# Optimization experiments

Hardware: AMD Instinct MI355X
Metric: run time of the kernel (lower is better)

## Reference

```python
import jax, jax.numpy as jnp
import numpy as np

N = 100000       # nodes
E = 1600000      # edges (before self loops)
G = 64           # graphs in batch
IN, HID, OUT = 128, 64, 16
NEG_SLOPE = 0.2  # PyG GATConv default


def setup_inputs() -> dict:
    key = jax.random.key(0)
    ks = jax.random.split(key, 16)
    s = 0.1  # weight init scale
    return {
        "x": jax.random.normal(ks[0], (N, IN), dtype=jnp.float32),
        "edge_index": jax.random.randint(ks[1], (2, E), 0, N, dtype=jnp.int32),
        "batch": jnp.sort(jax.random.randint(ks[2], (N,), 0, G, dtype=jnp.int32)),
        "W1": jax.random.normal(ks[3], (IN, 2 * HID), dtype=jnp.float32) * s,
        "a_src1": jax.random.normal(ks[4], (2, HID), dtype=jnp.float32) * s,
        "a_dst1": jax.random.normal(ks[5], (2, HID), dtype=jnp.float32) * s,
        "b1": jax.random.normal(ks[6], (2 * HID,), dtype=jnp.float32) * s,
        "W2": jax.random.normal(ks[7], (2 * HID, HID), dtype=jnp.float32) * s,
        "a_src2": jax.random.normal(ks[8], (1, HID), dtype=jnp.float32) * s,
        "a_dst2": jax.random.normal(ks[9], (1, HID), dtype=jnp.float32) * s,
        "b2": jax.random.normal(ks[10], (HID,), dtype=jnp.float32) * s,
        "dw1": jax.random.normal(ks[11], (HID, HID), dtype=jnp.float32) * s,
        "db1": jax.random.normal(ks[12], (HID,), dtype=jnp.float32) * s,
        "dw2": jax.random.normal(ks[13], (HID, OUT), dtype=jnp.float32) * s,
        "db2": jax.random.normal(ks[14], (OUT,), dtype=jnp.float32) * s,
    }


def gat_conv(x, src, dst, W, a_src, a_dst, b):
    """PyG GATConv (concat=True, self-loops already appended to src/dst)."""
    n = x.shape[0]
    heads, out = a_src.shape
    h = (x @ W).reshape(n, heads, out)                       # [N,H,O]
    e_src = jnp.einsum("nho,ho->nh", h, a_src)               # [N,H]
    e_dst = jnp.einsum("nho,ho->nh", h, a_dst)
    e = jax.nn.leaky_relu(e_src[src] + e_dst[dst], NEG_SLOPE)  # [E',H]
    # segment softmax over incoming edges of each destination node
    m = jax.lax.stop_gradient(jax.ops.segment_max(e, dst, num_segments=n))
    a = jnp.exp(e - m[dst])
    denom = jax.ops.segment_sum(a, dst, num_segments=n)
    alpha = a / denom[dst]                                   # [E',H]
    msg = h[src] * alpha[:, :, None]                         # [E',H,O]
    agg = jax.ops.segment_sum(msg, dst, num_segments=n)      # [N,H,O]
    return agg.reshape(n, heads * out) + b


def reference(x, edge_index, batch, W1, a_src1, a_dst1, b1, W2, a_src2, a_dst2,
              b2, dw1, db1, dw2, db2):
    n = x.shape[0]
    loops = jnp.arange(n, dtype=edge_index.dtype)            # add_self_loops=True
    src = jnp.concatenate([edge_index[0], loops])
    dst = jnp.concatenate([edge_index[1], loops])

    h = jax.nn.relu(gat_conv(x, src, dst, W1, a_src1, a_dst1, b1))   # [N,128]
    h = gat_conv(h, src, dst, W2, a_src2, a_dst2, b2)                # [N,64]

    # global mean pool over graphs
    cnt = jax.ops.segment_sum(jnp.ones((n,), h.dtype), batch, num_segments=G)
    pooled = jax.ops.segment_sum(h, batch, num_segments=G)
    pooled = pooled / jnp.maximum(cnt, 1.0)[:, None]                  # [G,64]

    # decoder MLP (dropout inactive in eval)
    z = jax.nn.relu(pooled @ dw1 + db1)
    return z @ dw2 + db2                                              # [G,16]
```

## Files before the change

### kernel.cpp

```cpp
#include <hip/hip_runtime.h>
#include <stdint.h>


#define LRELU(x) ((x) > 0.f ? (x) : 0.2f * (x))
#define LOG2E 1.4426950408889634f
#define BCAP 3072

typedef short bf8 __attribute__((ext_vector_type(8)));
typedef float f32x4 __attribute__((ext_vector_type(4)));
typedef float f32x2 __attribute__((ext_vector_type(2)));

__device__ __forceinline__ uint16_t f2bf(float f) {
  uint32_t u = __float_as_uint(f);
  u += 0x7fff + ((u >> 16) & 1);
  return (uint16_t)(u >> 16);
}
__device__ __forceinline__ uint32_t pack2bf(float a, float b) {
  return (uint32_t)f2bf(a) | ((uint32_t)f2bf(b) << 16);
}
__device__ __forceinline__ uint8_t f2fp8(float v) {
  return (uint8_t)(__builtin_amdgcn_cvt_pk_fp8_f32(v, v, 0, false) & 0xff);
}
__device__ __forceinline__ void fp8x4_to_f32(uint32_t v, float* o) {
  f32x2 lo = __builtin_amdgcn_cvt_pk_f32_fp8(v, false);
  f32x2 hi = __builtin_amdgcn_cvt_pk_f32_fp8(v, true);
  o[0] = lo[0]; o[1] = lo[1]; o[2] = hi[0]; o[3] = hi[1];
}


__global__ __launch_bounds__(256) void scatter_cvt_kernel(
    const int* __restrict__ ei, int* __restrict__ bcur,
    uint32_t* __restrict__ bpack, const float* __restrict__ W1,
    const float* __restrict__ W2, uint16_t* __restrict__ WT1,
    uint16_t* __restrict__ WT2, int E, int E2, int shift, int nb, int gCH) {
  int blk = blockIdx.x;
  int t = threadIdx.x;
  if (blk >= gCH) {
    int idx = (blk - gCH) * 256 + t;
    if (idx < 128 * 128) {
      int n = idx >> 7, k = idx & 127;
      WT1[idx] = f2bf(W1[(size_t)k * 128 + n]);
    } else if (idx < 128 * 128 + 64 * 128) {
      int j = idx - 128 * 128;
      int n = j >> 7, k = j & 127;
      WT2[j] = f2bf(W2[(size_t)k * 64 + n]);
    }
    return;
  }
  __shared__ int lh[1024];
  __shared__ int lb[1024];
  for (int i = t; i < 1024; i += 256) lh[i] = 0;
  __syncthreads();
  int base = blk * 4096;
  int bszm1 = (1 << shift) - 1;
  uint32_t pk[16];
  int rk[16], bk[16];
#pragma unroll
  for (int u = 0; u < 16; ++u) {
    int e = base + u * 256 + t;
    if (e < E2) {
      int s, d;
      if (e < E) { s = ei[e]; d = ei[E + e]; } else { s = d = e - E; }
      bk[u] = d >> shift;
      pk[u] = ((uint32_t)s << shift) | (uint32_t)(d & bszm1);
      rk[u] = atomicAdd(&lh[bk[u]], 1);
    } else rk[u] = -1;
  }
  __syncthreads();
  for (int i = t; i < nb; i += 256) {
    int c = lh[i];
    lb[i] = c ? atomicAdd(&bcur[i], c) : 0;
  }
  __syncthreads();
#pragma unroll
  for (int u = 0; u < 16; ++u) {
    if (rk[u] >= 0) {
      int pos = lb[bk[u]] + rk[u];
      if (pos < BCAP) bpack[(size_t)bk[u] * BCAP + pos] = pk[u];
    }
  }
}


__device__ __forceinline__ void bfinal_body(const uint32_t* __restrict__ bpack,
                                            const int* __restrict__ bcur,
                                            int2* __restrict__ off2,
                                            int* __restrict__ ssrc, int N,
                                            int shift, int b) {
  __shared__ int hist[512];
  __shared__ int loff[512];
  __shared__ int ssc[256];
  __shared__ int lsrc[BCAP];
  int t = threadIdx.x;
  int bsz = 1 << shift;
  int node0 = b << shift;
  int e0 = b * BCAP;
  int cnt = min(bcur[b], BCAP);
  for (int i = t; i < bsz; i += 256) hist[i] = 0;
  __syncthreads();
  uint32_t pe[12];
  int ne = 0;
#pragma unroll
  for (int j = 0; j < 12; ++j) {
    int i = j * 256 + t;
    if (i < cnt) { pe[j] = bpack[(size_t)b * BCAP + i]; ne = j + 1; }
  }
  int bszm1 = bsz - 1;
  for (int j = 0; j < ne; ++j) atomicAdd(&hist[pe[j] & bszm1], 1);
  __syncthreads();
  int per = (bsz + 255) >> 8;
  int basei = t * per;
  int va[2] = {0, 0};
  int sum = 0;
#pragma unroll 2
  for (int j = 0; j < per; ++j) {
    if (basei + j < bsz) va[j] = hist[basei + j];
    sum += va[j];
  }
  ssc[t] = sum;
  __syncthreads();
  for (int d = 1; d < 256; d <<= 1) {
    int x = (t >= d) ? ssc[t - d] : 0;
    __syncthreads();
    ssc[t] += x;
    __syncthreads();
  }
  int run = ssc[t] - sum;
#pragma unroll 2
  for (int j = 0; j < per; ++j) {
    if (basei + j < bsz) {
      loff[basei + j] = run;
      int v = node0 + basei + j;
      if (v < N) off2[v] = make_int2(e0 + run, e0 + run + va[j]);
      run += va[j];
    }
  }
  for (int i = t; i < bsz; i += 256) hist[i] = 0;
  __syncthreads();
  for (int j = 0; j < ne; ++j) {
    int ld = pe[j] & bszm1;
    int r = atomicAdd(&hist[ld], 1);
    lsrc[loff[ld] + r] = (int)(pe[j] >> shift);
  }
  __syncthreads();
  for (int i = t; i < cnt; i += 256) ssrc[e0 + i] = lsrc[i];
}


template <int N, int HEADS, int AFP32>
__device__ __forceinline__ void gemm_body(const void* __restrict__ Av,
                                          const uint16_t* __restrict__ WT,
                                          uint8_t* __restrict__ C,
                                          const float* __restrict__ aS,
                                          const float* __restrict__ aD,
                                          float* __restrict__ es,
                                          float* __restrict__ ed, int M, int blk) {
  constexpr int CT = N / 16;
  int wave = threadIdx.x >> 6;
  int lane = threadIdx.x & 63;
  int m16 = lane & 15;
  int quad = lane >> 4;
  int row_base = blk * 128 + wave * 32;
  if (row_base >= M) return;
  const uint16_t* Ab0 = (const uint16_t*)Av + (size_t)(row_base + m16) * 128;
  const uint16_t* Ab1 = Ab0 + (size_t)16 * 128;
  const float* Af0 = (const float*)Av + (size_t)(row_base + m16) * 128;
  const float* Af1 = Af0 + (size_t)16 * 128;
  f32x4 acc[2][CT] = {};
#pragma unroll
  for (int ks = 0; ks < 4; ++ks) {
    int k0 = ks * 32 + quad * 8;
    bf8 a0, a1;
    if (AFP32) {
      float4 v0 = *reinterpret_cast<const float4*>(Af0 + k0);
      float4 v1 = *reinterpret_cast<const float4*>(Af0 + k0 + 4);
      uint4 pk0;
      pk0.x = pack2bf(v0.x, v0.y); pk0.y = pack2bf(v0.z, v0.w);
      pk0.z = pack2bf(v1.x, v1.y); pk0.w = pack2bf(v1.z, v1.w);
      a0 = *reinterpret_cast<bf8*>(&pk0);
      float4 w0 = *reinterpret_cast<const float4*>(Af1 + k0);
      float4 w1 = *reinterpret_cast<const float4*>(Af1 + k0 + 4);
      uint4 pk1;
      pk1.x = pack2bf(w0.x, w0.y); pk1.y = pack2bf(w0.z, w0.w);
      pk1.z = pack2bf(w1.x, w1.y); pk1.w = pack2bf(w1.z, w1.w);
      a1 = *reinterpret_cast<bf8*>(&pk1);
    } else {
      a0 = *reinterpret_cast<const bf8*>(Ab0 + k0);
      a1 = *reinterpret_cast<const bf8*>(Ab1 + k0);
    }
#pragma unroll
    for (int c = 0; c < CT; ++c) {
      bf8 b = *reinterpret_cast<const bf8*>(WT + (size_t)(c * 16 + m16) * 128 + k0);
      acc[0][c] = __builtin_amdgcn_mfma_f32_16x16x32_bf16(a0, b, acc[0][c], 0, 0, 0);
      acc[1][c] = __builtin_amdgcn_mfma_f32_16x16x32_bf16(a1, b, acc[1][c], 0, 0, 0);
    }
  }
#pragma unroll
  for (int r = 0; r < 2; ++r) {
#pragma unroll
    for (int c = 0; c < CT; ++c) {
#pragma unroll
      for (int reg = 0; reg < 4; ++reg) {
        int row = row_base + r * 16 + quad * 4 + reg;
        C[(size_t)row * N + c * 16 + m16] = f2fp8(acc[r][c][reg]);
      }
    }
  }
  float aSv[CT], aDv[CT];
#pragma unroll
  for (int c = 0; c < CT; ++c) {
    aSv[c] = aS[c * 16 + m16];
    aDv[c] = aD[c * 16 + m16];
  }
#pragma unroll
  for (int r = 0; r < 2; ++r) {
#pragma unroll
    for (int reg = 0; reg < 4; ++reg) {
      float es0 = 0.f, es1 = 0.f, ed0 = 0.f, ed1 = 0.f;
#pragma unroll
      for (int c = 0; c < CT; ++c) {
        float v = acc[r][c][reg];
        if (HEADS == 2 && c >= CT / 2) {
          es1 = fmaf(v, aSv[c], es1);
          ed1 = fmaf(v, aDv[c], ed1);
        } else {
          es0 = fmaf(v, aSv[c], es0);
          ed0 = fmaf(v, aDv[c], ed0);
        }
      }
#pragma unroll
      for (int o = 1; o < 16; o <<= 1) {
        es0 += __shfl_xor(es0, o);
        ed0 += __shfl_xor(ed0, o);
        if (HEADS == 2) {
          es1 += __shfl_xor(es1, o);
          ed1 += __shfl_xor(ed1, o);
        }
      }
      if (m16 == 0) {
        int row = row_base + r * 16 + quad * 4 + reg;
        if (HEADS == 2) {
          es[row * 2] = es0 * LOG2E; es[row * 2 + 1] = es1 * LOG2E;
          ed[row * 2] = ed0 * LOG2E; ed[row * 2 + 1] = ed1 * LOG2E;
        } else {
          es[row] = es0 * LOG2E;
          ed[row] = ed0 * LOG2E;
        }
      }
    }
  }
}


__global__ __launch_bounds__(256) void gemm1_bfinal_kernel(
    const float* __restrict__ x, const uint16_t* __restrict__ WT1,
    uint8_t* __restrict__ hb1, const float* __restrict__ aS,
    const float* __restrict__ aD, float* __restrict__ es, float* __restrict__ ed,
    int M, const uint32_t* __restrict__ bpack, const int* __restrict__ bcur,
    int2* __restrict__ off2, int* __restrict__ ssrc, int shift, int gM) {
  int blk = blockIdx.x;
  if (blk < gM) {
    gemm_body<128, 2, 1>(x, WT1, hb1, aS, aD, es, ed, M, blk);
  } else {
    bfinal_body(bpack, bcur, off2, ssrc, M, shift, blk - gM);
  }
}

template <int N, int HEADS, int AFP32>
__global__ __launch_bounds__(256) void gemm_mfma(const void* __restrict__ Av,
                                                 const uint16_t* __restrict__ WT,
                                                 uint8_t* __restrict__ C,
                                                 const float* __restrict__ aS,
                                                 const float* __restrict__ aD,
                                                 float* __restrict__ es,
                                                 float* __restrict__ ed, int M) {
  gemm_body<N, HEADS, AFP32>(Av, WT, C, aS, aD, es, ed, M, blockIdx.x);
}


__global__ void agg1_kernel(const uint2* __restrict__ h8, const float* __restrict__ es,
                            const float2* __restrict__ ed, const int2* __restrict__ off2,
                            const int* __restrict__ ssrc, const float* __restrict__ b,
                            uint4* __restrict__ outb4, int n) {
  int w = __builtin_amdgcn_readfirstlane((blockIdx.x * 256 + threadIdx.x) >> 6);
  int lane = threadIdx.x & 63;
  if (w >= n) return;
  int sub = lane >> 4;
  int q = lane & 15;
  bool hi = q >= 8;
  float2 edw = ed[w];
  float edh = hi ? edw.y : edw.x;
  const float* esp = es + (hi ? 1 : 0);
  float acc[8] = {};
  float den = 0.f;
  int2 oo = off2[w];
  int e0 = oo.x, e1 = oo.y;
  int base = e0;
  for (; base + 8 <= e1; base += 8) {
    int s0 = ssrc[base + sub];
    int s1 = ssrc[base + 4 + sub];
    float ev0 = esp[2 * s0];
    float ev1 = esp[2 * s1];
    uint2 g0 = h8[(size_t)s0 * 16 + q];
    uint2 g1 = h8[(size_t)s1 * 16 + q];
    float a0 = exp2f(LRELU(ev0 + edh));
    float a1 = exp2f(LRELU(ev1 + edh));
    den += a0 + a1;
    float f0[8], f1[8];
    fp8x4_to_f32(g0.x, f0); fp8x4_to_f32(g0.y, f0 + 4);
    fp8x4_to_f32(g1.x, f1); fp8x4_to_f32(g1.y, f1 + 4);
#pragma unroll
    for (int j = 0; j < 8; ++j) acc[j] = fmaf(a0, f0[j], acc[j]);
#pragma unroll
    for (int j = 0; j < 8; ++j) acc[j] = fmaf(a1, f1[j], acc[j]);
  }
  if (base + 4 <= e1) {
    int s0 = ssrc[base + sub];
    float ev0 = esp[2 * s0];
    uint2 g0 = h8[(size_t)s0 * 16 + q];
    float a0 = exp2f(LRELU(ev0 + edh));
    den += a0;
    float f0[8];
    fp8x4_to_f32(g0.x, f0); fp8x4_to_f32(g0.y, f0 + 4);
#pragma unroll
    for (int j = 0; j < 8; ++j) acc[j] = fmaf(a0, f0[j], acc[j]);
    base += 4;
  }
  int e = base + sub;
  if (e < e1) {
    int s0 = ssrc[e];
    float ev0 = esp[2 * s0];
    uint2 g0 = h8[(size_t)s0 * 16 + q];
    float a0 = exp2f(LRELU(ev0 + edh));
    den += a0;
    float f0[8];
    fp8x4_to_f32(g0.x, f0); fp8x4_to_f32(g0.y, f0 + 4);
#pragma unroll
    for (int j = 0; j < 8; ++j) acc[j] = fmaf(a0, f0[j], acc[j]);
  }
#pragma unroll
  for (int m = 16; m <= 32; m <<= 1) {
    den += __shfl_xor(den, m);
#pragma unroll
    for (int j = 0; j < 8; ++j) acc[j] += __shfl_xor(acc[j], m);
  }
  if (sub == 0) {
    float inv = 1.0f / den;
    float4 b0 = reinterpret_cast<const float4*>(b)[q * 2];
    float4 b1 = reinterpret_cast<const float4*>(b)[q * 2 + 1];
    float o0 = fmaxf(fmaf(acc[0], inv, b0.x), 0.f);
    float o1 = fmaxf(fmaf(acc[1], inv, b0.y), 0.f);
    float o2 = fmaxf(fmaf(acc[2], inv, b0.z), 0.f);
    float o3 = fmaxf(fmaf(acc[3], inv, b0.w), 0.f);
    float o4 = fmaxf(fmaf(acc[4], inv, b1.x), 0.f);
    float o5 = fmaxf(fmaf(acc[5], inv, b1.y), 0.f);
    float o6 = fmaxf(fmaf(acc[6], inv, b1.z), 0.f);
    float o7 = fmaxf(fmaf(acc[7], inv, b1.w), 0.f);
    uint4 o;
    o.x = pack2bf(o0, o1);
    o.y = pack2bf(o2, o3);
    o.z = pack2bf(o4, o5);
    o.w = pack2bf(o6, o7);
    outb4[(size_t)w * 16 + q] = o;
  }
}


__global__ void agg2_pool_kernel(const uint32_t* __restrict__ h8,
                                 const float* __restrict__ es,
                                 const float* __restrict__ ed,
                                 const int2* __restrict__ off2,
                                 const int* __restrict__ ssrc,
                                 const float* __restrict__ b,
                                 const int* __restrict__ batch,
                                 float* __restrict__ pooled, int n) {
  int w = __builtin_amdgcn_readfirstlane((blockIdx.x * 256 + threadIdx.x) >> 6);
  int wave = threadIdx.x >> 6;
  int lane = threadIdx.x & 63;
  bool act = (w < n);
  int sub = lane >> 4;
  int q = lane & 15;
  __shared__ float red[4][64];
  __shared__ int gidS[4];
  float acc[4] = {};
  float den = 1.f;
  if (act) {
    float edw = ed[w];
    den = 0.f;
    int2 oo = off2[w];
    int e0 = oo.x, e1 = oo.y;
    int base = e0;
    for (; base + 8 <= e1; base += 8) {
      int s0 = ssrc[base + sub];
      int s1 = ssrc[base + 4 + sub];
      float ev0 = es[s0];
      float ev1 = es[s1];
      uint32_t g0 = h8[(size_t)s0 * 16 + q];
      uint32_t g1 = h8[(size_t)s1 * 16 + q];
      float a0 = exp2f(LRELU(ev0 + edw));
      float a1 = exp2f(LRELU(ev1 + edw));
      den += a0 + a1;
      float f0[4], f1[4];
      fp8x4_to_f32(g0, f0);
      fp8x4_to_f32(g1, f1);
#pragma unroll
      for (int j = 0; j < 4; ++j) acc[j] = fmaf(a0, f0[j], acc[j]);
#pragma unroll
      for (int j = 0; j < 4; ++j) acc[j] = fmaf(a1, f1[j], acc[j]);
    }
    if (base + 4 <= e1) {
      int s0 = ssrc[base + sub];
      float ev0 = es[s0];
      uint32_t g0 = h8[(size_t)s0 * 16 + q];
      float a0 = exp2f(LRELU(ev0 + edw));
      den += a0;
      float f0[4];
      fp8x4_to_f32(g0, f0);
#pragma unroll
      for (int j = 0; j < 4; ++j) acc[j] = fmaf(a0, f0[j], acc[j]);
      base += 4;
    }
    int e = base + sub;
    if (e < e1) {
      int s0 = ssrc[e];
      float ev0 = es[s0];
      uint32_t g0 = h8[(size_t)s0 * 16 + q];
      float a0 = exp2f(LRELU(ev0 + edw));
      den += a0;
      float f0[4];
      fp8x4_to_f32(g0, f0);
#pragma unroll
      for (int j = 0; j < 4; ++j) acc[j] = fmaf(a0, f0[j], acc[j]);
    }
#pragma unroll
    for (int m = 16; m <= 32; m <<= 1) {
      den += __shfl_xor(den, m);
#pragma unroll
      for (int j = 0; j < 4; ++j) acc[j] += __shfl_xor(acc[j], m);
    }
    if (sub == 0) {
      float inv = 1.0f / den;
      float4 bb = reinterpret_cast<const float4*>(b)[q];
      red[wave][q * 4 + 0] = fmaf(acc[0], inv, bb.x);
      red[wave][q * 4 + 1] = fmaf(acc[1], inv, bb.y);
      red[wave][q * 4 + 2] = fmaf(acc[2], inv, bb.z);
      red[wave][q * 4 + 3] = fmaf(acc[3], inv, bb.w);
    }
  }
  if (lane == 0) gidS[wave] = act ? batch[w] : -1;
  __syncthreads();
  int g0 = gidS[0];
  bool uni = (g0 >= 0) & (gidS[1] == g0) & (gidS[2] == g0) & (gidS[3] == g0);
  int t = threadIdx.x;
  if (uni) {
    if (t < 64) {
      float s = red[0][t] + red[1][t] + red[2][t] + red[3][t];
      atomicAdd(&pooled[g0 * 64 + t], s);
    }
  } else {
    int wv = t >> 6, c = t & 63;
    int g = gidS[wv];
    if (g >= 0) atomicAdd(&pooled[g * 64 + c], red[wv][c]);
  }
}


__device__ __forceinline__ int lowerb(const int* __restrict__ a, int n, int v) {
  int lo = 0, hi = n;
  while (lo < hi) {
    int mid = (lo + hi) >> 1;
    if (a[mid] < v) lo = mid + 1; else hi = mid;
  }
  return lo;
}

__global__ void mlp_kernel(const float* __restrict__ pooled,
                           const int* __restrict__ batch, int n,
                           const float* __restrict__ dw1, const float* __restrict__ db1,
                           const float* __restrict__ dw2, const float* __restrict__ db2,
                           float* __restrict__ out) {
  int g = blockIdx.x;
  int c = threadIdx.x;
  __shared__ float P[64];
  __shared__ float Z[64];
  __shared__ int cntS;
  if (c == 0) cntS = lowerb(batch, n, g + 1) - lowerb(batch, n, g);
  __syncthreads();
  float inv = 1.0f / fmaxf((float)cntS, 1.0f);
  P[c] = pooled[g * 64 + c] * inv;
  __syncthreads();
  float s = db1[c];
#pragma unroll
  for (int k = 0; k < 64; ++k) s = fmaf(P[k], dw1[k * 64 + c], s);
  Z[c] = fmaxf(s, 0.f);
  __syncthreads();
  if (c < 16) {
    float s2 = db2[c];
#pragma unroll
    for (int k = 0; k < 64; ++k) s2 = fmaf(Z[k], dw2[k * 16 + c], s2);
    out[g * 16 + c] = s2;
  }
}


extern "C" void kernel_launch(void* const* d_in, const int* in_sizes, int n_in,
                              void* d_out, int out_size, void* d_ws, size_t ws_size,
                              hipStream_t stream) {
  const float* x      = (const float*)d_in[0];
  const int*   ei     = (const int*)d_in[1];
  const int*   batch  = (const int*)d_in[2];
  const float* W1     = (const float*)d_in[3];
  const float* a_src1 = (const float*)d_in[4];
  const float* a_dst1 = (const float*)d_in[5];
  const float* b1     = (const float*)d_in[6];
  const float* W2     = (const float*)d_in[7];
  const float* a_src2 = (const float*)d_in[8];
  const float* a_dst2 = (const float*)d_in[9];
  const float* b2     = (const float*)d_in[10];
  const float* dw1    = (const float*)d_in[11];
  const float* db1    = (const float*)d_in[12];
  const float* dw2    = (const float*)d_in[13];
  const float* db2    = (const float*)d_in[14];
  float* out = (float*)d_out;

  const int N = in_sizes[2];
  const int E = in_sizes[1] / 2;
  const int E2 = E + N;
  const int G = out_size / 16;

  int shift = 7;
  while ((N >> shift) >= 1024) ++shift;
  const int NB = ((N - 1) >> shift) + 1;

  char* ws = (char*)d_ws;
  size_t o = 0;
  auto alloc = [&](size_t bytes) {
    void* p = ws + o;
    o = (o + bytes + 255) & ~(size_t)255;
    return p;
  };
  int*      zreg   = (int*)alloc((size_t)(1024 + G * 64) * 4);
  int*      bcur   = zreg;
  float*    pooled = (float*)(zreg + 1024);
  int2*     off2   = (int2*)alloc((size_t)N * 8);
  uint32_t* bpack  = (uint32_t*)alloc((size_t)NB * BCAP * 4);
  int*      ssrc   = (int*)alloc((size_t)NB * BCAP * 4);
  float*    es1    = (float*)alloc((size_t)N * 2 * 4);
  float*    ed1    = (float*)alloc((size_t)N * 2 * 4);
  float*    es2    = (float*)alloc((size_t)N * 4);
  float*    ed2    = (float*)alloc((size_t)N * 4);
  uint16_t* wt1b   = (uint16_t*)alloc((size_t)128 * 128 * 2);
  uint16_t* wt2b   = (uint16_t*)alloc((size_t)64 * 128 * 2);
  uint8_t*  hb1    = (uint8_t*)alloc((size_t)N * 128);
  uint8_t*  hb2    = (uint8_t*)alloc((size_t)N * 64);
  uint32_t* out1b  = (uint32_t*)alloc((size_t)N * 64 * 4);

  hipMemsetAsync(zreg, 0, (size_t)(1024 + G * 64) * 4, stream);

  int gM   = (N + 127) / 128;
  int gW   = (N + 3) / 4;
  int gCH  = (E2 + 4095) / 4096;
  int gCVT = (128 * 128 + 64 * 128 + 255) / 256;

  scatter_cvt_kernel<<<gCH + gCVT, 256, 0, stream>>>(ei, bcur, bpack, W1, W2,
                                                     wt1b, wt2b, E, E2, shift,
                                                     NB, gCH);
  gemm1_bfinal_kernel<<<gM + NB, 256, 0, stream>>>(x, wt1b, hb1, a_src1, a_dst1,
                                                   es1, ed1, N, bpack, bcur,
                                                   off2, ssrc, shift, gM);
  agg1_kernel<<<gW, 256, 0, stream>>>((const uint2*)hb1, es1,
                                      (const float2*)ed1, off2, ssrc, b1,
                                      (uint4*)out1b, N);
  gemm_mfma<64, 1, 0><<<gM, 256, 0, stream>>>((const void*)out1b, wt2b, hb2,
                                              a_src2, a_dst2, es2, ed2, N);
  agg2_pool_kernel<<<gW, 256, 0, stream>>>((const uint32_t*)hb2, es2, ed2, off2,
                                           ssrc, b2, batch, pooled, N);
  mlp_kernel<<<G, 64, 0, stream>>>(pooled, batch, N, dw1, db1, dw2, db2, out);
}
```

Measured before the change: 312.7 us.

## Widen per-lane gathers in aggregation kernels and slice pooled atomics

Both aggregation kernels now use 8 lanes per edge with 16-byte (layer 1) or 8-byte (layer 2) fp8 gathers, so each wave processes 8 edges at once instead of 4 and issues fewer, wider loads. The pooled sum is spread across 8 slices indexed by block id, which cuts atomic contention on the 64x64 accumulator, and the MLP kernel adds the slices back together. In exchange each lane holds more accumulator registers, the shuffle reduction takes one more step, and the memset and final pooled read grow eightfold.

```diff
diff --git a/kernel.cpp b/kernel.cpp
--- a/kernel.cpp
+++ b/kernel.cpp
@@ -5,6 +5,7 @@
 #define LRELU(x) ((x) > 0.f ? (x) : 0.2f * (x))
 #define LOG2E 1.4426950408889634f
 #define BCAP 3072
+#define PSLICE 8
 
 typedef short bf8 __attribute__((ext_vector_type(8)));
 typedef float f32x4 __attribute__((ext_vector_type(4)));
@@ -278,111 +279,115 @@
 }
 
 
-__global__ void agg1_kernel(const uint2* __restrict__ h8, const float* __restrict__ es,
+__global__ void agg1_kernel(const uint4* __restrict__ h16, const float* __restrict__ es,
                             const float2* __restrict__ ed, const int2* __restrict__ off2,
                             const int* __restrict__ ssrc, const float* __restrict__ b,
                             uint4* __restrict__ outb4, int n) {
   int w = __builtin_amdgcn_readfirstlane((blockIdx.x * 256 + threadIdx.x) >> 6);
   int lane = threadIdx.x & 63;
   if (w >= n) return;
-  int sub = lane >> 4;
-  int q = lane & 15;
-  bool hi = q >= 8;
+  int sub = lane >> 3;
+  int q = lane & 7;
+  bool hi = q >= 4;
   float2 edw = ed[w];
   float edh = hi ? edw.y : edw.x;
   const float* esp = es + (hi ? 1 : 0);
-  float acc[8] = {};
+  float acc[16] = {};
   float den = 0.f;
   int2 oo = off2[w];
   int e0 = oo.x, e1 = oo.y;
   int base = e0;
-  for (; base + 8 <= e1; base += 8) {
+  for (; base + 16 <= e1; base += 16) {
     int s0 = ssrc[base + sub];
-    int s1 = ssrc[base + 4 + sub];
+    int s1 = ssrc[base + 8 + sub];
     float ev0 = esp[2 * s0];
     float ev1 = esp[2 * s1];
-    uint2 g0 = h8[(size_t)s0 * 16 + q];
-    uint2 g1 = h8[(size_t)s1 * 16 + q];
+    uint4 g0 = h16[(size_t)s0 * 8 + q];
+    uint4 g1 = h16[(size_t)s1 * 8 + q];
     float a0 = exp2f(LRELU(ev0 + edh));
     float a1 = exp2f(LRELU(ev1 + edh));
     den += a0 + a1;
-    float f0[8], f1[8];
+    float f0[16], f1[16];
     fp8x4_to_f32(g0.x, f0); fp8x4_to_f32(g0.y, f0 + 4);
+    fp8x4_to_f32(g0.z, f0 + 8); fp8x4_to_f32(g0.w, f0 + 12);
     fp8x4_to_f32(g1.x, f1); fp8x4_to_f32(g1.y, f1 + 4);
-#pragma unroll
-    for (int j = 0; j < 8; ++j) acc[j] = fmaf(a0, f0[j], acc[j]);
-#pragma unroll
-    for (int j = 0; j < 8; ++j) acc[j] = fmaf(a1, f1[j], acc[j]);
-  }
-  if (base + 4 <= e1) {
+    fp8x4_to_f32(g1.z, f1 + 8); fp8x4_to_f32(g1.w, f1 + 12);
+#pragma unroll
+    for (int j = 0; j < 16; ++j) acc[j] = fmaf(a0, f0[j], acc[j]);
+#pragma unroll
+    for (int j = 0; j < 16; ++j) acc[j] = fmaf(a1, f1[j], acc[j]);
+  }
+  if (base + 8 <= e1) {
     int s0 = ssrc[base + sub];
     float ev0 = esp[2 * s0];
-    uint2 g0 = h8[(size_t)s0 * 16 + q];
+    uint4 g0 = h16[(size_t)s0 * 8 + q];
     float a0 = exp2f(LRELU(ev0 + edh));
     den += a0;
-    float f0[8];
+    float f0[16];
     fp8x4_to_f32(g0.x, f0); fp8x4_to_f32(g0.y, f0 + 4);
-#pragma unroll
-    for (int j = 0; j < 8; ++j) acc[j] = fmaf(a0, f0[j], acc[j]);
-    base += 4;
+    fp8x4_to_f32(g0.z, f0 + 8); fp8x4_to_f32(g0.w, f0 + 12);
+#pragma unroll
+    for (int j = 0; j < 16; ++j) acc[j] = fmaf(a0, f0[j], acc[j]);
+    base += 8;
   }
   int e = base + sub;
   if (e < e1) {
     int s0 = ssrc[e];
     float ev0 = esp[2 * s0];
-    uint2 g0 = h8[(size_t)s0 * 16 + q];
+    uint4 g0 = h16[(size_t)s0 * 8 + q];
     float a0 = exp2f(LRELU(ev0 + edh));
     den += a0;
-    float f0[8];
+    float f0[16];
     fp8x4_to_f32(g0.x, f0); fp8x4_to_f32(g0.y, f0 + 4);
-#pragma unroll
-    for (int j = 0; j < 8; ++j) acc[j] = fmaf(a0, f0[j], acc[j]);
-  }
-#pragma unroll
-  for (int m = 16; m <= 32; m <<= 1) {
+    fp8x4_to_f32(g0.z, f0 + 8); fp8x4_to_f32(g0.w, f0 + 12);
+#pragma unroll
+    for (int j = 0; j < 16; ++j) acc[j] = fmaf(a0, f0[j], acc[j]);
+  }
+#pragma unroll
+  for (int m = 8; m <= 32; m <<= 1) {
     den += __shfl_xor(den, m);
 #pragma unroll
-    for (int j = 0; j < 8; ++j) acc[j] += __shfl_xor(acc[j], m);
+    for (int j = 0; j < 16; ++j) acc[j] += __shfl_xor(acc[j], m);
   }
   if (sub == 0) {
     float inv = 1.0f / den;
-    float4 b0 = reinterpret_cast<const float4*>(b)[q * 2];
-    float4 b1 = reinterpret_cast<const float4*>(b)[q * 2 + 1];
-    float o0 = fmaxf(fmaf(acc[0], inv, b0.x), 0.f);
-    float o1 = fmaxf(fmaf(acc[1], inv, b0.y), 0.f);
-    float o2 = fmaxf(fmaf(acc[2], inv, b0.z), 0.f);
-    float o3 = fmaxf(fmaf(acc[3], inv, b0.w), 0.f);
-    float o4 = fmaxf(fmaf(acc[4], inv, b1.x), 0.f);
-    float o5 = fmaxf(fmaf(acc[5], inv, b1.y), 0.f);
-    float o6 = fmaxf(fmaf(acc[6], inv, b1.z), 0.f);
-    float o7 = fmaxf(fmaf(acc[7], inv, b1.w), 0.f);
-    uint4 o;
-    o.x = pack2bf(o0, o1);
-    o.y = pack2bf(o2, o3);
-    o.z = pack2bf(o4, o5);
-    o.w = pack2bf(o6, o7);
-    outb4[(size_t)w * 16 + q] = o;
-  }
-}
-
-
-__global__ void agg2_pool_kernel(const uint32_t* __restrict__ h8,
+    float o[16];
+#pragma unroll
+    for (int k = 0; k < 4; ++k) {
+      float4 bb = reinterpret_cast<const float4*>(b)[q * 4 + k];
+      o[k * 4 + 0] = fmaxf(fmaf(acc[k * 4 + 0], inv, bb.x), 0.f);
+      o[k * 4 + 1] = fmaxf(fmaf(acc[k * 4 + 1], inv, bb.y), 0.f);
+      o[k * 4 + 2] = fmaxf(fmaf(acc[k * 4 + 2], inv, bb.z), 0.f);
+      o[k * 4 + 3] = fmaxf(fmaf(acc[k * 4 + 3], inv, bb.w), 0.f);
+    }
+    uint4 oA, oB;
+    oA.x = pack2bf(o[0], o[1]);   oA.y = pack2bf(o[2], o[3]);
+    oA.z = pack2bf(o[4], o[5]);   oA.w = pack2bf(o[6], o[7]);
+    oB.x = pack2bf(o[8], o[9]);   oB.y = pack2bf(o[10], o[11]);
+    oB.z = pack2bf(o[12], o[13]); oB.w = pack2bf(o[14], o[15]);
+    outb4[(size_t)w * 16 + q * 2] = oA;
+    outb4[(size_t)w * 16 + q * 2 + 1] = oB;
+  }
+}
+
+
+__global__ void agg2_pool_kernel(const uint2* __restrict__ h8,
                                  const float* __restrict__ es,
                                  const float* __restrict__ ed,
                                  const int2* __restrict__ off2,
                                  const int* __restrict__ ssrc,
                                  const float* __restrict__ b,
                                  const int* __restrict__ batch,
-                                 float* __restrict__ pooled, int n) {
+                                 float* __restrict__ pooled, int gstride, int n) {
   int w = __builtin_amdgcn_readfirstlane((blockIdx.x * 256 + threadIdx.x) >> 6);
   int wave = threadIdx.x >> 6;
   int lane = threadIdx.x & 63;
   bool act = (w < n);
-  int sub = lane >> 4;
-  int q = lane & 15;
+  int sub = lane >> 3;
+  int q = lane & 7;
   __shared__ float red[4][64];
   __shared__ int gidS[4];
-  float acc[4] = {};
+  float acc[8] = {};
   float den = 1.f;
   if (act) {
     float edw = ed[w];
@@ -390,77 +395,83 @@
     int2 oo = off2[w];
     int e0 = oo.x, e1 = oo.y;
     int base = e0;
-    for (; base + 8 <= e1; base += 8) {
+    for (; base + 16 <= e1; base += 16) {
       int s0 = ssrc[base + sub];
-      int s1 = ssrc[base + 4 + sub];
+      int s1 = ssrc[base + 8 + sub];
       float ev0 = es[s0];
       float ev1 = es[s1];
-      uint32_t g0 = h8[(size_t)s0 * 16 + q];
-      uint32_t g1 = h8[(size_t)s1 * 16 + q];
+      uint2 g0 = h8[(size_t)s0 * 8 + q];
+      uint2 g1 = h8[(size_t)s1 * 8 + q];
       float a0 = exp2f(LRELU(ev0 + edw));
       float a1 = exp2f(LRELU(ev1 + edw));
       den += a0 + a1;
-      float f0[4], f1[4];
-      fp8x4_to_f32(g0, f0);
-      fp8x4_to_f32(g1, f1);
-#pragma unroll
-      for (int j = 0; j < 4; ++j) acc[j] = fmaf(a0, f0[j], acc[j]);
-#pragma unroll
-      for (int j = 0; j < 4; ++j) acc[j] = fmaf(a1, f1[j], acc[j]);
-    }
-    if (base + 4 <= e1) {
+      float f0[8], f1[8];
+      fp8x4_to_f32(g0.x, f0); fp8x4_to_f32(g0.y, f0 + 4);
+      fp8x4_to_f32(g1.x, f1); fp8x4_to_f32(g1.y, f1 + 4);
+#pragma unroll
+      for (int j = 0; j < 8; ++j) acc[j] = fmaf(a0, f0[j], acc[j]);
+#pragma unroll
+      for (int j = 0; j < 8; ++j) acc[j] = fmaf(a1, f1[j], acc[j]);
+    }
+    if (base + 8 <= e1) {
       int s0 = ssrc[base + sub];
       float ev0 = es[s0];
-      uint32_t g0 = h8[(size_t)s0 * 16 + q];
+      uint2 g0 = h8[(size_t)s0 * 8 + q];
       float a0 = exp2f(LRELU(ev0 + edw));
       den += a0;
-      float f0[4];
-      fp8x4_to_f32(g0, f0);
-#pragma unroll
-      for (int j = 0; j < 4; ++j) acc[j] = fmaf(a0, f0[j], acc[j]);
-      base += 4;
+      float f0[8];
+      fp8x4_to_f32(g0.x, f0); fp8x4_to_f32(g0.y, f0 + 4);
+#pragma unroll
+      for (int j = 0; j < 8; ++j) acc[j] = fmaf(a0, f0[j], acc[j]);
+      base += 8;
     }
     int e = base + sub;
     if (e < e1) {
       int s0 = ssrc[e];
       float ev0 = es[s0];
-      uint32_t g0 = h8[(size_t)s0 * 16 + q];
+      uint2 g0 = h8[(size_t)s0 * 8 + q];
       float a0 = exp2f(LRELU(ev0 + edw));
       den += a0;
-      float f0[4];
-      fp8x4_to_f32(g0, f0);
-#pragma unroll
-      for (int j = 0; j < 4; ++j) acc[j] = fmaf(a0, f0[j], acc[j]);
-    }
-#pragma unroll
-    for (int m = 16; m <= 32; m <<= 1) {
+      float f0[8];
+      fp8x4_to_f32(g0.x, f0); fp8x4_to_f32(g0.y, f0 + 4);
+#pragma unroll
+      for (int j = 0; j < 8; ++j) acc[j] = fmaf(a0, f0[j], acc[j]);
+    }
+#pragma unroll
+    for (int m = 8; m <= 32; m <<= 1) {
       den += __shfl_xor(den, m);
 #pragma unroll
-      for (int j = 0; j < 4; ++j) acc[j] += __shfl_xor(acc[j], m);
+      for (int j = 0; j < 8; ++j) acc[j] += __shfl_xor(acc[j], m);
     }
     if (sub == 0) {
       float inv = 1.0f / den;
-      float4 bb = reinterpret_cast<const float4*>(b)[q];
-      red[wave][q * 4 + 0] = fmaf(acc[0], inv, bb.x);
-      red[wave][q * 4 + 1] = fmaf(acc[1], inv, bb.y);
-      red[wave][q * 4 + 2] = fmaf(acc[2], inv, bb.z);
-      red[wave][q * 4 + 3] = fmaf(acc[3], inv, bb.w);
+      float4 b0 = reinterpret_cast<const float4*>(b)[q * 2];
+      float4 b1 = reinterpret_cast<const float4*>(b)[q * 2 + 1];
+      red[wave][q * 8 + 0] = fmaf(acc[0], inv, b0.x);
+      red[wave][q * 8 + 1] = fmaf(acc[1], inv, b0.y);
+      red[wave][q * 8 + 2] = fmaf(acc[2], inv, b0.z);
+      red[wave][q * 8 + 3] = fmaf(acc[3], inv, b0.w);
+      red[wave][q * 8 + 4] = fmaf(acc[4], inv, b1.x);
+      red[wave][q * 8 + 5] = fmaf(acc[5], inv, b1.y);
+      red[wave][q * 8 + 6] = fmaf(acc[6], inv, b1.z);
+      red[wave][q * 8 + 7] = fmaf(acc[7], inv, b1.w);
     }
   }
   if (lane == 0) gidS[wave] = act ? batch[w] : -1;
   __syncthreads();
+  float* pslice = pooled + (size_t)(blockIdx.x & (PSLICE - 1)) * gstride;
   int g0 = gidS[0];
   bool uni = (g0 >= 0) & (gidS[1] == g0) & (gidS[2] == g0) & (gidS[3] == g0);
   int t = threadIdx.x;
   if (uni) {
     if (t < 64) {
       float s = red[0][t] + red[1][t] + red[2][t] + red[3][t];
-      atomicAdd(&pooled[g0 * 64 + t], s);
+      atomicAdd(&pslice[g0 * 64 + t], s);
     }
   } else {
     int wv = t >> 6, c = t & 63;
     int g = gidS[wv];
-    if (g >= 0) atomicAdd(&pooled[g * 64 + c], red[wv][c]);
+    if (g >= 0) atomicAdd(&pslice[g * 64 + c], red[wv][c]);
   }
 }
 
@@ -474,7 +485,7 @@
   return lo;
 }
 
-__global__ void mlp_kernel(const float* __restrict__ pooled,
+__global__ void mlp_kernel(const float* __restrict__ pooled, int gstride,
                            const int* __restrict__ batch, int n,
                            const float* __restrict__ dw1, const float* __restrict__ db1,
                            const float* __restrict__ dw2, const float* __restrict__ db2,
@@ -487,7 +498,10 @@
   if (c == 0) cntS = lowerb(batch, n, g + 1) - lowerb(batch, n, g);
   __syncthreads();
   float inv = 1.0f / fmaxf((float)cntS, 1.0f);
-  P[c] = pooled[g * 64 + c] * inv;
+  float p = 0.f;
+#pragma unroll
+  for (int s = 0; s < PSLICE; ++s) p += pooled[(size_t)s * gstride + g * 64 + c];
+  P[c] = p * inv;
   __syncthreads();
   float s = db1[c];
 #pragma unroll
@@ -527,6 +541,7 @@
   const int E = in_sizes[1] / 2;
   const int E2 = E + N;
   const int G = out_size / 16;
+  const int gstride = G * 64;
 
   int shift = 7;
   while ((N >> shift) >= 1024) ++shift;
@@ -539,7 +554,7 @@
     o = (o + bytes + 255) & ~(size_t)255;
     return p;
   };
-  int*      zreg   = (int*)alloc((size_t)(1024 + G * 64) * 4);
+  int*      zreg   = (int*)alloc((size_t)(1024 + PSLICE * gstride) * 4);
   int*      bcur   = zreg;
   float*    pooled = (float*)(zreg + 1024);
   int2*     off2   = (int2*)alloc((size_t)N * 8);
@@ -555,7 +570,7 @@
   uint8_t*  hb2    = (uint8_t*)alloc((size_t)N * 64);
   uint32_t* out1b  = (uint32_t*)alloc((size_t)N * 64 * 4);
 
-  hipMemsetAsync(zreg, 0, (size_t)(1024 + G * 64) * 4, stream);
+  hipMemsetAsync(zreg, 0, (size_t)(1024 + PSLICE * gstride) * 4, stream);
 
   int gM   = (N + 127) / 128;
   int gW   = (N + 3) / 4;
@@ -568,12 +583,13 @@
   gemm1_bfinal_kernel<<<gM + NB, 256, 0, stream>>>(x, wt1b, hb1, a_src1, a_dst1,
                                                    es1, ed1, N, bpack, bcur,
                                                    off2, ssrc, shift, gM);
-  agg1_kernel<<<gW, 256, 0, stream>>>((const uint2*)hb1, es1,
+  agg1_kernel<<<gW, 256, 0, stream>>>((const uint4*)hb1, es1,
                                       (const float2*)ed1, off2, ssrc, b1,
                                       (uint4*)out1b, N);
   gemm_mfma<64, 1, 0><<<gM, 256, 0, stream>>>((const void*)out1b, wt2b, hb2,
                                               a_src2, a_dst2, es2, ed2, N);
-  agg2_pool_kernel<<<gW, 256, 0, stream>>>((const uint32_t*)hb2, es2, ed2, off2,
-                                           ssrc, b2, batch, pooled, N);
-  mlp_kernel<<<G, 64, 0, stream>>>(pooled, batch, N, dw1, db1, dw2, db2, out);
-}
+  agg2_pool_kernel<<<gW, 256, 0, stream>>>((const uint2*)hb2, es2, ed2, off2,
+                                           ssrc, b2, batch, pooled, gstride, N);
+  mlp_kernel<<<G, 64, 0, stream>>>(pooled, gstride, batch, N, dw1, db1, dw2,
+                                   db2, out);
+}
```

After: 309.7 us. About the same (-1.0%).
